# Optimization experiments

Hardware: AMD Instinct MI355X
Metric: run time of the kernel (lower is better)

The kernel has to match this reference:

```python
import jax, jax.numpy as jnp
import numpy as np

D = 256; H = 8; DK = D // H
NT, NW, ND = 2000, 50000, 20000
E_TT, E_WT, E_TD, E_WD = 128000, 256000, 320000, 320000
SQRT_DK = float(np.sqrt(DK))


def setup_inputs() -> dict:
    key = jax.random.key(0)
    ks = jax.random.split(key, 32)
    def nrm(i, shape, s=0.05):
        return jax.random.normal(ks[i], shape, jnp.float32) * s
    inp = {
        "feat_topic": nrm(0, (NT, D), 1.0),
        "feat_word": nrm(1, (NW, D), 1.0),
        "feat_doc": nrm(2, (ND, D), 1.0),
        "ht_prev": nrm(3, (NT, D), 1.0),
        # stacked per-ntype linears, index: 0=topic, 1=word, 2=doc
        "Wk": nrm(4, (3, D, D)), "bk": nrm(5, (3, D)),
        "Wq": nrm(6, (3, D, D)), "bq": nrm(7, (3, D)),
        "Wv": nrm(8, (3, D, D)), "bv": nrm(9, (3, D)),
        # a_linears, index: 0=topic, 1=doc
        "Wa": nrm(10, (2, D, D)), "ba": nrm(11, (2, D)),
        "ln_g": jnp.ones((2, D), jnp.float32),
        "ln_b": jnp.zeros((2, D), jnp.float32),
        "skip": jnp.ones((2,), jnp.float32),
        # RNNCell for topic
        "Wih": nrm(12, (D, D)), "Whh": nrm(13, (D, D)),
        "bih": nrm(14, (D,)), "bhh": nrm(15, (D,)),
        # relation params, index: 0=tt, 1=wt, 2=td, 3=wd
        "rel_pri": jnp.ones((4, H), jnp.float32),
        "rel_att": nrm(16, (4, H, DK, DK), 0.1),
        "rel_msg": nrm(17, (4, H, DK, DK), 0.1),
        "src_tt": jax.random.randint(ks[18], (E_TT,), 0, NT),
        "dst_tt": jnp.arange(E_TT, dtype=jnp.int32) % NT,
        "src_wt": jax.random.randint(ks[19], (E_WT,), 0, NW),
        "dst_wt": jnp.arange(E_WT, dtype=jnp.int32) % NT,
        "src_td": jax.random.randint(ks[20], (E_TD,), 0, NT),
        "dst_td": jnp.arange(E_TD, dtype=jnp.int32) % ND,
        "src_wd": jax.random.randint(ks[21], (E_WD,), 0, NW),
        "dst_wd": jnp.arange(E_WD, dtype=jnp.int32) % ND,
    }
    return inp


def _proj(x, W, b):
    return (x @ W + b).reshape(-1, H, DK)


def _layernorm(x, g, b):
    mu = x.mean(-1, keepdims=True)
    var = ((x - mu) ** 2).mean(-1, keepdims=True)
    return (x - mu) * jax.lax.rsqrt(var + 1e-5) * g + b


def _rel_message(k, v, q, src, dst, pri, A_att, A_msg, n_dst):
    # k,v: [N_src,H,DK]; q: [N_dst,H,DK]; per-edge gather-compute-scatter
    key = jnp.einsum('ehd,hdo->eho', k[src], A_att)          # [E,H,DK]
    att = (q[dst] * key).sum(-1) * pri / SQRT_DK             # [E,H]
    val = jnp.einsum('ehd,hdo->eho', v[src], A_msg)          # [E,H,DK]
    m = jax.ops.segment_max(att, dst, num_segments=n_dst)
    e = jnp.exp(att - m[dst])
    s = jax.ops.segment_sum(e, dst, num_segments=n_dst)
    a = e / s[dst]                                           # edge softmax per dst
    t = jax.ops.segment_sum(a[..., None] * val, dst, num_segments=n_dst)
    return jax.nn.relu(t.reshape(n_dst, D))


def reference(feat_topic, feat_word, feat_doc, ht_prev, Wk, bk, Wq, bq, Wv, bv,
              Wa, ba, ln_g, ln_b, skip, Wih, Whh, bih, bhh,
              rel_pri, rel_att, rel_msg,
              src_tt, dst_tt, src_wt, dst_wt, src_td, dst_td, src_wd, dst_wd):
    # ---- phase 1: messages into topic nodes (etypes tt, wt) ----
    k_t = _proj(feat_topic, Wk[0], bk[0]); v_t = _proj(feat_topic, Wv[0], bv[0])
    k_w = _proj(feat_word,  Wk[1], bk[1]); v_w = _proj(feat_word,  Wv[1], bv[1])
    q_t = _proj(feat_topic, Wq[0], bq[0])
    t_tt = _rel_message(k_t, v_t, q_t, src_tt, dst_tt, rel_pri[0], rel_att[0], rel_msg[0], NT)
    t_wt = _rel_message(k_w, v_w, q_t, src_wt, dst_wt, rel_pri[1], rel_att[1], rel_msg[1], NT)
    t_topic = 0.5 * (t_tt + t_wt)                            # cross_reducer='mean'
    alpha = jax.nn.sigmoid(skip[0])
    trans = t_topic @ Wa[0] + ba[0]
    mix = trans * alpha + feat_topic * (1.0 - alpha)
    h = jnp.tanh(mix @ Wih + bih + ht_prev @ Whh + bhh)      # RNNCell
    topic_out = _layernorm(h, ln_g[0], ln_b[0])
    # ---- phase 2: messages into doc nodes (etypes td, wd), topic uses updated feats ----
    k_t2 = _proj(topic_out, Wk[0], bk[0]); v_t2 = _proj(topic_out, Wv[0], bv[0])
    q_d = _proj(feat_doc, Wq[2], bq[2])
    t_td = _rel_message(k_t2, v_t2, q_d, src_td, dst_td, rel_pri[2], rel_att[2], rel_msg[2], ND)
    t_wd = _rel_message(k_w, v_w, q_d, src_wd, dst_wd, rel_pri[3], rel_att[3], rel_msg[3], ND)
    t_doc = 0.5 * (t_td + t_wd)
    alpha2 = jax.nn.sigmoid(skip[1])
    trans2 = t_doc @ Wa[1] + ba[1]
    mix2 = trans2 * alpha2 + feat_doc * (1.0 - alpha2)
    doc_out = _layernorm(mix2, ln_g[1], ln_b[1])
    return topic_out, doc_out
```

## Files before the change

### kernel.cpp

```cpp
#include <hip/hip_runtime.h>
#include <hip/hip_bf16.h>
#include <hip/hip_fp8.h>

typedef __attribute__((ext_vector_type(8))) short bf16x8;
typedef __attribute__((ext_vector_type(4))) float f32x4;
typedef __attribute__((ext_vector_type(2))) float f32x2;

constexpr int NT = 2000, NW = 50000, ND = 20000;
constexpr float INV_SQRT_DK = 0.17677669529663687f;

__device__ inline float bfu(unsigned short u) {
    return __uint_as_float(((unsigned int)u) << 16);
}
__device__ inline float blo(unsigned int u) { return __uint_as_float(u << 16); }
__device__ inline float bhi(unsigned int u) { return __uint_as_float(u & 0xffff0000u); }
__device__ inline short f2bf(float x) {
    __hip_bfloat16 h = __float2bfloat16(x);
    short s; __builtin_memcpy(&s, &h, 2); return s;
}

__device__ inline void dec4(unsigned int w, float* o) {
#if __has_builtin(__builtin_amdgcn_cvt_pk_f32_fp8)
    f32x2 a = __builtin_amdgcn_cvt_pk_f32_fp8(w, false);
    f32x2 b = __builtin_amdgcn_cvt_pk_f32_fp8(w, true);
    o[0] = a[0]; o[1] = a[1]; o[2] = b[0]; o[3] = b[1];
#else
    __hip_fp8_e4m3 t0, t1, t2, t3;
    t0.__x = (__hip_fp8_storage_t)(w & 0xff);
    t1.__x = (__hip_fp8_storage_t)((w >> 8) & 0xff);
    t2.__x = (__hip_fp8_storage_t)((w >> 16) & 0xff);
    t3.__x = (__hip_fp8_storage_t)((w >> 24) & 0xff);
    o[0] = (float)t0; o[1] = (float)t1; o[2] = (float)t2; o[3] = (float)t3;
#endif
}
__device__ inline unsigned char f2fp8(float v) {
#if __has_builtin(__builtin_amdgcn_cvt_pk_fp8_f32)
    return (unsigned char)(__builtin_amdgcn_cvt_pk_fp8_f32(v, v, 0u, false) & 0xff);
#else
    __hip_fp8_e4m3 h(v); return (unsigned char)h.__x;
#endif
}

__device__ inline void cstore(float* p, float v) { *p = v; }
__device__ inline void cstore(short* p, float v) { *p = f2bf(v); }
__device__ inline void cstore(unsigned char* p, float v) { *p = f2fp8(v); }

__device__ inline void cstore4(float* p, float4 v) {
    *reinterpret_cast<float4*>(p) = v;
}
__device__ inline void cstore4(short* p, float4 v) {
    short4 s; s.x = f2bf(v.x); s.y = f2bf(v.y); s.z = f2bf(v.z); s.w = f2bf(v.w);
    *reinterpret_cast<short4*>(p) = s;
}
__device__ inline void cstore4(unsigned char* p, float4 v) {
#if __has_builtin(__builtin_amdgcn_cvt_pk_fp8_f32)
    unsigned int w = __builtin_amdgcn_cvt_pk_fp8_f32(v.x, v.y, 0u, false);
    w = __builtin_amdgcn_cvt_pk_fp8_f32(v.z, v.w, w, true);
    *reinterpret_cast<unsigned int*>(p) = w;
#else
    p[0] = f2fp8(v.x); p[1] = f2fp8(v.y); p[2] = f2fp8(v.z); p[3] = f2fp8(v.w);
#endif
}

__device__ inline void gload16(const short* g, short* l) {
    __builtin_amdgcn_global_load_lds(
        (const __attribute__((address_space(1))) void*)g,
        (__attribute__((address_space(3))) void*)l, 16, 0, 0);
}

__device__ inline float dot32f8(const unsigned char* __restrict__ kp, const float* __restrict__ qh) {
    const uint4 u = *reinterpret_cast<const uint4*>(kp);
    const uint4 v = *reinterpret_cast<const uint4*>(kp + 16);
    const unsigned int ws[8] = {u.x, u.y, u.z, u.w, v.x, v.y, v.z, v.w};
    float d = 0.f;
    #pragma unroll
    for (int c = 0; c < 8; ++c) {
        float f[4];
        dec4(ws[c], f);
        d += qh[c * 4 + 0] * f[0] + qh[c * 4 + 1] * f[1]
           + qh[c * 4 + 2] * f[2] + qh[c * 4 + 3] * f[3];
    }
    return d;
}

__global__ __launch_bounds__(256) void fold_kernel(
    const float* __restrict__ Wk, const float* __restrict__ bk,
    const float* __restrict__ Wv, const float* __restrict__ bv,
    const float* __restrict__ rel_att, const float* __restrict__ rel_msg,
    short* __restrict__ B_t1, short* __restrict__ B_w, short* __restrict__ B_t2,
    float* __restrict__ bias_t1, float* __restrict__ bias_w, float* __restrict__ bias_t2)
{
    const int f = blockIdx.x >> 3, chunk = blockIdx.x & 7;
    const int rel = f >> 1, isV = f & 1;
    const int ntype = (rel == 1 || rel == 3) ? 1 : 0;
    const float* Wsrc = (isV ? Wv : Wk) + ntype * 65536;
    const float* bsrc = (isV ? bv : bk) + ntype * 256;
    const float* A    = (isV ? rel_msg : rel_att) + rel * 8192;
    short* wdst; float* bdst;
    switch (f) {
        case 0: wdst = B_t1 + 65536;     bdst = bias_t1 + 256; break;
        case 1: wdst = B_t1 + 2 * 65536; bdst = bias_t1 + 512; break;
        case 2: wdst = B_w;              bdst = bias_w;        break;
        case 3: wdst = B_w + 65536;      bdst = bias_w + 256;  break;
        case 4: wdst = B_t2;             bdst = bias_t2;       break;
        case 5: wdst = B_t2 + 65536;     bdst = bias_t2 + 256; break;
        case 6: wdst = B_w + 2 * 65536;  bdst = bias_w + 512;  break;
        default: wdst = B_w + 3 * 65536; bdst = bias_w + 768;  break;
    }
    __shared__ float Wsh[32][256];
    const int tid = threadIdx.x;
    for (int i = 0; i < 32; ++i)
        Wsh[i][tid] = Wsrc[(chunk * 32 + i) * 256 + tid];
    __syncthreads();
    const int h = tid >> 5, o = tid & 31;
    float a[32];
    #pragma unroll
    for (int d = 0; d < 32; ++d) a[d] = A[h * 1024 + d * 32 + o];
    short tmp[32];
    #pragma unroll
    for (int r = 0; r < 32; ++r) {
        float s = 0.f;
        #pragma unroll
        for (int d = 0; d < 32; ++d) s = fmaf(Wsh[r][(h << 5) + d], a[d], s);
        tmp[r] = f2bf(s);
    }
    short* wp = wdst + tid * 256 + chunk * 32;
    #pragma unroll
    for (int r8 = 0; r8 < 4; ++r8) {
        bf16x8 v;
        #pragma unroll
        for (int t = 0; t < 8; ++t) v[t] = tmp[r8 * 8 + t];
        *reinterpret_cast<bf16x8*>(wp + r8 * 8) = v;
    }
    if (chunk == 0) {
        float s = 0.f;
        #pragma unroll
        for (int d = 0; d < 32; ++d) s = fmaf(bsrc[(h << 5) + d], a[d], s);
        bdst[tid] = s;
    }
}

struct TransP { const float* s[6]; short* d[6]; };
__global__ __launch_bounds__(256) void wtrans6(TransP p) {
    const int m = blockIdx.y, n = blockIdx.x, k = threadIdx.x;
    p.d[m][n * 256 + k] = f2bf(p.s[m][k * 256 + n]);
}

__global__ void copy_bias(const float* __restrict__ s, float* __restrict__ d) {
    d[threadIdx.x] = s[threadIdx.x];
}

template <typename OutT, int EPI, int NI>
__device__ inline void epilogue(
    f32x4 (&acc)[NI][4], const float* __restrict__ bias, OutT* __restrict__ C,
    int M, int ldc, const float* __restrict__ extra,
    const float* __restrict__ skipv, int skipIdx,
    int row0, int col0, int wm, int wn, int r, int kb)
{
    float alpha = 0.f;
    if (EPI == 1) alpha = 1.f / (1.f + __expf(-skipv[skipIdx]));
    float4 b4[4];
    #pragma unroll
    for (int j = 0; j < 4; ++j)
        b4[j] = *reinterpret_cast<const float4*>(&bias[col0 + wn * 64 + j * 16 + kb * 4]);
    #pragma unroll
    for (int i = 0; i < NI; ++i) {
        const int rrow = row0 + wm * 64 + i * 16 + r;
        if (rrow >= M) continue;
        #pragma unroll
        for (int j = 0; j < 4; ++j) {
            const int cb = col0 + wn * 64 + j * 16 + kb * 4;
            float4 v;
            v.x = acc[i][j][0] + b4[j].x;
            v.y = acc[i][j][1] + b4[j].y;
            v.z = acc[i][j][2] + b4[j].z;
            v.w = acc[i][j][3] + b4[j].w;
            if (EPI == 1) {
                const float4 e = *reinterpret_cast<const float4*>(&extra[rrow * 256 + cb]);
                v.x = alpha * v.x + (1.f - alpha) * e.x;
                v.y = alpha * v.y + (1.f - alpha) * e.y;
                v.z = alpha * v.z + (1.f - alpha) * e.z;
                v.w = alpha * v.w + (1.f - alpha) * e.w;
            }
            if (EPI == 2) {
                const float4 e = *reinterpret_cast<const float4*>(&extra[rrow * 256 + cb]);
                v.x = tanhf(v.x + e.x);
                v.y = tanhf(v.y + e.y);
                v.z = tanhf(v.z + e.z);
                v.w = tanhf(v.w + e.w);
            }
            cstore4(C + rrow * ldc + cb, v);
        }
    }
}

template <bool XF32, typename OutT, int EPI, bool SWZ>
__global__ __launch_bounds__(256) void gemm_lds(
    const void* __restrict__ Xv, const short* __restrict__ Wt,
    const float* __restrict__ bias, OutT* __restrict__ C,
    int M, int ldc, const float* __restrict__ extra,
    const float* __restrict__ skipv, int skipIdx)
{
    __shared__ short As[128 * 64];
    __shared__ short Bs[128 * 64];
    int bxi = blockIdx.x, byi = blockIdx.y;
    if constexpr (SWZ) {
        const int h = bxi + (int)gridDim.x * byi;
        const int i = h >> 3;
        byi = (h & 7) + 8 * (i >> 3);
        bxi = i & 7;
        if (byi * 128 >= M) return;
    }
    const int tid = threadIdx.x;
    const int wave = tid >> 6, lane = tid & 63;
    const int wm = wave >> 1, wn = wave & 1;
    const int r = lane & 15, kb = lane >> 4;
    const int col0 = bxi * 128;
    const int row0 = byi * 128;

    const int l8 = lane >> 3;
    const int c8 = lane & 7;
    const int swz8 = c8 ^ l8;
    f32x4 acc[4][4] = {};

    for (int k0 = 0; k0 < 256; k0 += 64) {
        if (k0) __syncthreads();
        if constexpr (XF32) {
            #pragma unroll
            for (int q = 0; q < 4; ++q) {
                const int rl = wave * 32 + q * 8 + l8;
                const int grow = min(row0 + rl, M - 1);
                const float* xp = (const float*)Xv + grow * 256 + k0 + c8 * 8;
                const float4 x0 = *reinterpret_cast<const float4*>(xp);
                const float4 x1 = *reinterpret_cast<const float4*>(xp + 4);
                bf16x8 v;
                v[0] = f2bf(x0.x); v[1] = f2bf(x0.y); v[2] = f2bf(x0.z); v[3] = f2bf(x0.w);
                v[4] = f2bf(x1.x); v[5] = f2bf(x1.y); v[6] = f2bf(x1.z); v[7] = f2bf(x1.w);
                *reinterpret_cast<bf16x8*>(As + rl * 64 + swz8 * 8) = v;
            }
        } else {
            #pragma unroll
            for (int q = 0; q < 4; ++q) {
                const int rl = wave * 32 + q * 8 + l8;
                const int grow = min(row0 + rl, M - 1);
                gload16((const short*)Xv + grow * 256 + k0 + swz8 * 8,
                        As + (wave * 32 + q * 8) * 64);
            }
        }
        #pragma unroll
        for (int q = 0; q < 4; ++q) {
            const int cl = wave * 32 + q * 8 + l8;
            gload16(Wt + (col0 + cl) * 256 + k0 + swz8 * 8,
                    Bs + (wave * 32 + q * 8) * 64);
        }
        __syncthreads();
        #pragma unroll
        for (int s = 0; s < 2; ++s) {
            const int csw = ((kb + 4 * s) ^ (r & 7)) * 8;
            bf16x8 af[4], bw[4];
            #pragma unroll
            for (int i = 0; i < 4; ++i) {
                af[i] = *reinterpret_cast<const bf16x8*>(As + (wm * 64 + i * 16 + r) * 64 + csw);
                bw[i] = *reinterpret_cast<const bf16x8*>(Bs + (wn * 64 + i * 16 + r) * 64 + csw);
            }
            #pragma unroll
            for (int i = 0; i < 4; ++i)
                #pragma unroll
                for (int j = 0; j < 4; ++j)
                    acc[i][j] = __builtin_amdgcn_mfma_f32_16x16x32_bf16(bw[j], af[i], acc[i][j], 0, 0, 0);
        }
    }
    epilogue<OutT, EPI, 4>(acc, bias, C, M, ldc, extra, skipv, skipIdx,
                           row0, col0, wm, wn, r, kb);
}

__global__ __launch_bounds__(256) void gemm_qkv(
    const float* __restrict__ X, const short* __restrict__ Wt,
    const float* __restrict__ bias, short* __restrict__ Qo,
    unsigned char* __restrict__ KVo, int M)
{
    __shared__ short As[128 * 64];
    __shared__ short Bs[128 * 64];
    const int bxi = blockIdx.x, byi = blockIdx.y;
    const int tid = threadIdx.x;
    const int wave = tid >> 6, lane = tid & 63;
    const int wm = wave >> 1, wn = wave & 1;
    const int r = lane & 15, kb = lane >> 4;
    const int col0 = bxi * 128;
    const int row0 = byi * 128;

    const int l8 = lane >> 3;
    const int c8 = lane & 7;
    const int swz8 = c8 ^ l8;
    f32x4 acc[4][4] = {};

    for (int k0 = 0; k0 < 256; k0 += 64) {
        if (k0) __syncthreads();
        #pragma unroll
        for (int q = 0; q < 4; ++q) {
            const int rl = wave * 32 + q * 8 + l8;
            const int grow = min(row0 + rl, M - 1);
            const float* xp = X + grow * 256 + k0 + c8 * 8;
            const float4 x0 = *reinterpret_cast<const float4*>(xp);
            const float4 x1 = *reinterpret_cast<const float4*>(xp + 4);
            bf16x8 v;
            v[0] = f2bf(x0.x); v[1] = f2bf(x0.y); v[2] = f2bf(x0.z); v[3] = f2bf(x0.w);
            v[4] = f2bf(x1.x); v[5] = f2bf(x1.y); v[6] = f2bf(x1.z); v[7] = f2bf(x1.w);
            *reinterpret_cast<bf16x8*>(As + rl * 64 + swz8 * 8) = v;
        }
        #pragma unroll
        for (int q = 0; q < 4; ++q) {
            const int cl = wave * 32 + q * 8 + l8;
            gload16(Wt + (col0 + cl) * 256 + k0 + swz8 * 8,
                    Bs + (wave * 32 + q * 8) * 64);
        }
        __syncthreads();
        #pragma unroll
        for (int s = 0; s < 2; ++s) {
            const int csw = ((kb + 4 * s) ^ (r & 7)) * 8;
            bf16x8 af[4], bw[4];
            #pragma unroll
            for (int i = 0; i < 4; ++i) {
                af[i] = *reinterpret_cast<const bf16x8*>(As + (wm * 64 + i * 16 + r) * 64 + csw);
                bw[i] = *reinterpret_cast<const bf16x8*>(Bs + (wn * 64 + i * 16 + r) * 64 + csw);
            }
            #pragma unroll
            for (int i = 0; i < 4; ++i)
                #pragma unroll
                for (int j = 0; j < 4; ++j)
                    acc[i][j] = __builtin_amdgcn_mfma_f32_16x16x32_bf16(bw[j], af[i], acc[i][j], 0, 0, 0);
        }
    }

    float4 b4[4];
    #pragma unroll
    for (int j = 0; j < 4; ++j)
        b4[j] = *reinterpret_cast<const float4*>(&bias[col0 + wn * 64 + j * 16 + kb * 4]);
    #pragma unroll
    for (int i = 0; i < 4; ++i) {
        const int rrow = row0 + wm * 64 + i * 16 + r;
        if (rrow >= M) continue;
        #pragma unroll
        for (int j = 0; j < 4; ++j) {
            const int cb = col0 + wn * 64 + j * 16 + kb * 4;
            float4 v;
            v.x = acc[i][j][0] + b4[j].x;
            v.y = acc[i][j][1] + b4[j].y;
            v.z = acc[i][j][2] + b4[j].z;
            v.w = acc[i][j][3] + b4[j].w;
            if (bxi < 2) cstore4(Qo + rrow * 256 + cb, v);
            else         cstore4(KVo + rrow * 512 + (cb - 256), v);
        }
    }
}

template <bool XF32, typename OutT, int EPI, bool SWZ, bool SWAP>
__global__ __launch_bounds__(512) void gemm_w(
    const void* __restrict__ Xv, const short* __restrict__ Wt,
    const float* __restrict__ bias, OutT* __restrict__ C,
    int M, int ldc, const float* __restrict__ extra,
    const float* __restrict__ skipv, int skipIdx)
{
    __shared__ short As[256 * 64];
    __shared__ short Bs[128 * 64];
    int bxi = blockIdx.x, byi = blockIdx.y;
    if constexpr (SWZ) {
        const int h = bxi + (int)gridDim.x * byi;
        const int i = h >> 3;
        byi = (h & 7) + 8 * (i >> 3);
        bxi = i & 7;
        if (byi * 256 >= M) return;
    }
    const int tid = threadIdx.x;
    const int wave = tid >> 6, lane = tid & 63;
    const int wm = wave >> 1, wn = wave & 1;
    const int r = lane & 15, kb = lane >> 4;
    const int col0 = bxi * 128;
    const int row0 = byi * 256;

    const int l8 = lane >> 3;
    const int c8 = lane & 7;
    const int swz8 = c8 ^ l8;
    f32x4 acc[4][4] = {};

    for (int k0 = 0; k0 < 256; k0 += 64) {
        if (k0) __syncthreads();
        if constexpr (XF32) {
            #pragma unroll
            for (int q = 0; q < 4; ++q) {
                const int rl = wave * 32 + q * 8 + l8;
                const int grow = min(row0 + rl, M - 1);
                const float* xp = (const float*)Xv + grow * 256 + k0 + c8 * 8;
                const float4 x0 = *reinterpret_cast<const float4*>(xp);
                const float4 x1 = *reinterpret_cast<const float4*>(xp + 4);
                bf16x8 v;
                v[0] = f2bf(x0.x); v[1] = f2bf(x0.y); v[2] = f2bf(x0.z); v[3] = f2bf(x0.w);
                v[4] = f2bf(x1.x); v[5] = f2bf(x1.y); v[6] = f2bf(x1.z); v[7] = f2bf(x1.w);
                *reinterpret_cast<bf16x8*>(As + rl * 64 + swz8 * 8) = v;
            }
        } else {
            #pragma unroll
            for (int q = 0; q < 4; ++q) {
                const int rl = wave * 32 + q * 8 + l8;
                const int grow = min(row0 + rl, M - 1);
                gload16((const short*)Xv + grow * 256 + k0 + swz8 * 8,
                        As + (wave * 32 + q * 8) * 64);
            }
        }
        #pragma unroll
        for (int q = 0; q < 2; ++q) {
            const int cl = wave * 16 + q * 8 + l8;
            gload16(Wt + (col0 + cl) * 256 + k0 + swz8 * 8,
                    Bs + (wave * 16 + q * 8) * 64);
        }
        __syncthreads();
        #pragma unroll
        for (int s = 0; s < 2; ++s) {
            const int csw = ((kb + 4 * s) ^ (r & 7)) * 8;
            bf16x8 af[4], bw[4];
            #pragma unroll
            for (int i = 0; i < 4; ++i) {
                af[i] = *reinterpret_cast<const bf16x8*>(As + (wm * 64 + i * 16 + r) * 64 + csw);
                bw[i] = *reinterpret_cast<const bf16x8*>(Bs + (wn * 64 + i * 16 + r) * 64 + csw);
            }
            #pragma unroll
            for (int i = 0; i < 4; ++i)
                #pragma unroll
                for (int j = 0; j < 4; ++j) {
                    if constexpr (SWAP)
                        acc[i][j] = __builtin_amdgcn_mfma_f32_16x16x32_bf16(bw[j], af[i], acc[i][j], 0, 0, 0);
                    else
                        acc[i][j] = __builtin_amdgcn_mfma_f32_16x16x32_bf16(af[i], bw[j], acc[i][j], 0, 0, 0);
                }
        }
    }

    if constexpr (SWAP) {
        epilogue<OutT, EPI, 4>(acc, bias, C, M, ldc, extra, skipv, skipIdx,
                               row0, col0, wm, wn, r, kb);
    } else {
        float alpha = 0.f;
        if (EPI == 1) alpha = 1.f / (1.f + __expf(-skipv[skipIdx]));
        #pragma unroll
        for (int i = 0; i < 4; ++i) {
            #pragma unroll
            for (int j = 0; j < 4; ++j) {
                const int col = col0 + wn * 64 + j * 16 + r;
                const float bc = bias[col];
                #pragma unroll
                for (int t = 0; t < 4; ++t) {
                    const int rrow = row0 + wm * 64 + i * 16 + kb * 4 + t;
                    if (rrow < M) {
                        float v = acc[i][j][t] + bc;
                        if (EPI == 1) v = alpha * v + (1.f - alpha) * extra[rrow * 256 + col];
                        if (EPI == 2) v = tanhf(v + extra[rrow * 256 + col]);
                        cstore(C + rrow * ldc + col, v);
                    }
                }
            }
        }
    }
}

template <int NE>
__device__ inline void rel_scores_f8(const unsigned char* __restrict__ kv, int ld, int koff,
                                     const int* __restrict__ sidx, int off, float scale,
                                     const float* __restrict__ qh, float* __restrict__ sc,
                                     int g, int l)
{
    constexpr int NL = NE / 32;
    float att[NL];
    #pragma unroll
    for (int t = 0; t < NL; ++t)
        att[t] = dot32f8(kv + (size_t)sidx[off + l + 32 * t] * ld + koff + g * 32, qh) * scale;
    float m = att[0];
    #pragma unroll
    for (int t = 1; t < NL; ++t) m = fmaxf(m, att[t]);
    #pragma unroll
    for (int o = 16; o > 0; o >>= 1) m = fmaxf(m, __shfl_xor(m, o));
    float ex[NL], s = 0.f;
    #pragma unroll
    for (int t = 0; t < NL; ++t) { ex[t] = __expf(att[t] - m); s += ex[t]; }
    #pragma unroll
    for (int o = 16; o > 0; o >>= 1) s += __shfl_xor(s, o);
    const float inv = 1.f / s;
    #pragma unroll
    for (int t = 0; t < NL; ++t) sc[(off + l + 32 * t) * 9 + g] = ex[t] * inv;
}

template <int NEA, int NEB>
__global__ __launch_bounds__(256) void msg_k(
    const short* __restrict__ q, int ldq,
    const unsigned char* __restrict__ kvA, int ldA, int koffA, int voffA,
    const int* __restrict__ srcA,
    const unsigned char* __restrict__ kvB, int ldB, int koffB, int voffB,
    const int* __restrict__ srcB,
    const float* __restrict__ relPri, int relA, int relB,
    short* __restrict__ out, int n_dst)
{
    constexpr int NET = NEA + NEB;
    const int j = blockIdx.x, tid = threadIdx.x;
    __shared__ float qsh[256];
    __shared__ int sidx[NET];
    __shared__ float sc[NET * 9];
    __shared__ float ps[8][544];

    if (tid < 64) {
        const ushort4 u = *reinterpret_cast<const ushort4*>(
            (const unsigned short*)q + j * ldq + tid * 4);
        float4 f; f.x = bfu(u.x); f.y = bfu(u.y); f.z = bfu(u.z); f.w = bfu(u.w);
        *reinterpret_cast<float4*>(qsh + tid * 4) = f;
    }
    if (tid < NEA) sidx[tid] = srcA[j + tid * n_dst];
    else if (tid < NET) sidx[tid] = srcB[j + (tid - NEA) * n_dst];
    __syncthreads();

    const int g = tid >> 5, l = tid & 31;
    float qr[32];
    #pragma unroll
    for (int c = 0; c < 8; ++c) {
        const float4 v = *reinterpret_cast<const float4*>(qsh + g * 32 + c * 4);
        qr[c * 4] = v.x; qr[c * 4 + 1] = v.y; qr[c * 4 + 2] = v.z; qr[c * 4 + 3] = v.w;
    }

    if constexpr (NEA == 16 && NEB == 16) {
        const int isB = l >> 4;
        const unsigned char* base = isB ? kvB + koffB : kvA + koffA;
        const int ld = isB ? ldB : ldA;
        const float scale = relPri[(isB ? relB : relA) * 8 + g] * INV_SQRT_DK;
        const float att = dot32f8(base + (size_t)sidx[l] * ld + g * 32, qr) * scale;
        float m = att;
        #pragma unroll
        for (int o = 8; o > 0; o >>= 1) m = fmaxf(m, __shfl_xor(m, o));
        const float ex = __expf(att - m);
        float s = ex;
        #pragma unroll
        for (int o = 8; o > 0; o >>= 1) s += __shfl_xor(s, o);
        sc[l * 9 + g] = ex / s;
    } else {
        rel_scores_f8<NEA>(kvA, ldA, koffA, sidx, 0,
                           relPri[relA * 8 + g] * INV_SQRT_DK, qr, sc, g, l);
        rel_scores_f8<NEB>(kvB, ldB, koffB, sidx, NEA,
                           relPri[relB * 8 + g] * INV_SQRT_DK, qr, sc, g, l);
    }
    __syncthreads();

    const int ct16 = tid & 15;
    const int rel  = (tid >> 4) & 1;
    const int es   = tid >> 5;
    const int hh   = ct16 >> 1;
    const unsigned char* kvR = rel ? kvB : kvA;
    const int ldR   = rel ? ldB : ldA;
    const int voffR = rel ? voffB : voffA;
    const int offR  = rel ? NEA : 0;
    const int neR   = rel ? NEB : NEA;
    float acc[16] = {};
    for (int e = es; e < neR; e += 8) {
        const float w = sc[(offR + e) * 9 + hh];
        const uint4 u = *reinterpret_cast<const uint4*>(
            kvR + (size_t)sidx[offR + e] * ldR + voffR + ct16 * 16);
        float f[16];
        dec4(u.x, f); dec4(u.y, f + 4); dec4(u.z, f + 8); dec4(u.w, f + 12);
        #pragma unroll
        for (int k = 0; k < 16; ++k) acc[k] = fmaf(w, f[k], acc[k]);
    }
    {
        float* pp = &ps[es][rel * 272 + ct16 * 17];
        #pragma unroll
        for (int k = 0; k < 16; ++k) pp[k] = acc[k];
    }
    __syncthreads();

    const int ra = (tid >> 4) * 17 + (tid & 15);
    float rA = 0.f, rB = 0.f;
    #pragma unroll
    for (int e2 = 0; e2 < 8; ++e2) { rA += ps[e2][ra]; rB += ps[e2][272 + ra]; }
    const float val = 0.5f * (fmaxf(rA, 0.f) + fmaxf(rB, 0.f));
    unsigned short* ob = (unsigned short*)qsh;
    ob[tid] = (unsigned short)f2bf(val);
    __syncthreads();
    if (tid < 32) {
        const uint4 u = *reinterpret_cast<const uint4*>(ob + tid * 8);
        *reinterpret_cast<uint4*>((unsigned short*)out + j * 256 + tid * 8) = u;
    }
}

template <bool WB>
__global__ __launch_bounds__(256) void ln_k(
    float* __restrict__ data, const float* __restrict__ g,
    const float* __restrict__ b, int nrows, short* __restrict__ bfout)
{
    const int wid = threadIdx.x >> 6, lane = threadIdx.x & 63;
    const int row = blockIdx.x * 4 + wid;
    if (row >= nrows) return;
    float4 x = *reinterpret_cast<float4*>(data + row * 256 + lane * 4);
    float s  = x.x + x.y + x.z + x.w;
    float q2 = x.x * x.x + x.y * x.y + x.z * x.z + x.w * x.w;
    #pragma unroll
    for (int o = 32; o > 0; o >>= 1) { s += __shfl_xor(s, o); q2 += __shfl_xor(q2, o); }
    const float mu  = s * (1.f / 256.f);
    const float var = q2 * (1.f / 256.f) - mu * mu;
    const float rr = rsqrtf(var + 1e-5f);
    const float4 gg = *reinterpret_cast<const float4*>(g + lane * 4);
    const float4 bb = *reinterpret_cast<const float4*>(b + lane * 4);
    x.x = (x.x - mu) * rr * gg.x + bb.x;
    x.y = (x.y - mu) * rr * gg.y + bb.y;
    x.z = (x.z - mu) * rr * gg.z + bb.z;
    x.w = (x.w - mu) * rr * gg.w + bb.w;
    *reinterpret_cast<float4*>(data + row * 256 + lane * 4) = x;
    if (WB) {
        ushort4 u;
        u.x = (unsigned short)f2bf(x.x); u.y = (unsigned short)f2bf(x.y);
        u.z = (unsigned short)f2bf(x.z); u.w = (unsigned short)f2bf(x.w);
        *reinterpret_cast<ushort4*>((unsigned short*)bfout + row * 256 + lane * 4) = u;
    }
}

extern "C" void kernel_launch(void* const* d_in, const int* in_sizes, int n_in,
                              void* d_out, int out_size, void* d_ws, size_t ws_size,
                              hipStream_t stream)
{
    const float* feat_topic = (const float*)d_in[0];
    const float* feat_word  = (const float*)d_in[1];
    const float* feat_doc   = (const float*)d_in[2];
    const float* ht_prev    = (const float*)d_in[3];
    const float* Wk  = (const float*)d_in[4];
    const float* bk  = (const float*)d_in[5];
    const float* Wq  = (const float*)d_in[6];
    const float* bq  = (const float*)d_in[7];
    const float* Wv  = (const float*)d_in[8];
    const float* bv  = (const float*)d_in[9];
    const float* Wa  = (const float*)d_in[10];
    const float* ba  = (const float*)d_in[11];
    const float* ln_g = (const float*)d_in[12];
    const float* ln_b = (const float*)d_in[13];
    const float* skip = (const float*)d_in[14];
    const float* Wih  = (const float*)d_in[15];
    const float* Whh  = (const float*)d_in[16];
    const float* bih  = (const float*)d_in[17];
    const float* bhh  = (const float*)d_in[18];
    const float* rel_pri = (const float*)d_in[19];
    const float* rel_att = (const float*)d_in[20];
    const float* rel_msg = (const float*)d_in[21];
    const int* src_tt = (const int*)d_in[22];
    const int* src_wt = (const int*)d_in[24];
    const int* src_td = (const int*)d_in[26];
    const int* src_wd = (const int*)d_in[28];

    short* B_t1 = (short*)d_ws;
    short* B_w  = B_t1 + 196608;
    short* B_t2 = B_w + 262144;
    short* Wq2t = B_t2 + 131072;
    short* Whht = Wq2t + 65536;
    short* Wa0t = Whht + 65536;
    short* Wiht = Wa0t + 65536;
    short* Wa1t = Wiht + 65536;
    short* q_t  = Wa1t + 65536;
    unsigned char* kv1 = (unsigned char*)(q_t + 512000);
    unsigned char* w8  = kv1 + 1024000;
    unsigned char* kv2 = w8 + 51200000;
    short* qd   = (short*)(kv2 + 1024000);
    short* ttop = qd + 5120000;
    short* mixb = ttop + 512000;
    short* tdoc = mixb + 512000;
    short* xt2  = tdoc + 5120000;
    float* bias_t1 = (float*)(xt2 + 512000);
    float* bias_w  = bias_t1 + 768;
    float* bias_t2 = bias_w + 1024;
    float* r2      = bias_t2 + 512;

    float* out_topic = (float*)d_out;
    float* out_doc   = out_topic + NT * 256;

    fold_kernel<<<dim3(64), 256, 0, stream>>>(Wk, bk, Wv, bv, rel_att, rel_msg,
                                              B_t1, B_w, B_t2, bias_t1, bias_w, bias_t2);
    TransP tp;
    tp.s[0] = Wq;            tp.d[0] = B_t1;
    tp.s[1] = Wq + 131072;   tp.d[1] = Wq2t;
    tp.s[2] = Whh;           tp.d[2] = Whht;
    tp.s[3] = Wih;           tp.d[3] = Wiht;
    tp.s[4] = Wa;            tp.d[4] = Wa0t;
    tp.s[5] = Wa + 65536;    tp.d[5] = Wa1t;
    wtrans6<<<dim3(256, 6), 256, 0, stream>>>(tp);
    copy_bias<<<dim3(1), 256, 0, stream>>>(bq, bias_t1);

    gemm_w<true, unsigned char, 0, true, false><<<dim3(8, 200), 512, 0, stream>>>(
        feat_word, B_w, bias_w, w8, NW, 1024, nullptr, nullptr, 0);

    gemm_qkv<<<dim3(6, 16), 256, 0, stream>>>(
        feat_topic, B_t1, bias_t1, q_t, kv1, NT);
    gemm_w<true, short, 0, false, true><<<dim3(2, 79), 512, 0, stream>>>(
        feat_doc, Wq2t, bq + 512, qd, ND, 256, nullptr, nullptr, 0);
    gemm_lds<true, float, 0, false><<<dim3(2, 16), 256, 0, stream>>>(
        ht_prev, Whht, bhh, r2, NT, 256, nullptr, nullptr, 0);

    msg_k<64, 128><<<dim3(NT), 256, 0, stream>>>(
        q_t, 256,
        kv1, 512, 0, 256, src_tt,
        w8, 1024, 0, 256, src_wt,
        rel_pri, 0, 1, ttop, NT);

    gemm_lds<false, short, 1, false><<<dim3(2, 16), 256, 0, stream>>>(
        ttop, Wa0t, ba, mixb, NT, 256, feat_topic, skip, 0);
    gemm_lds<false, float, 2, false><<<dim3(2, 16), 256, 0, stream>>>(
        mixb, Wiht, bih, out_topic, NT, 256, r2, nullptr, 0);
    ln_k<true><<<dim3(500), 256, 0, stream>>>(out_topic, ln_g, ln_b, NT, xt2);

    gemm_lds<false, unsigned char, 0, false><<<dim3(4, 16), 256, 0, stream>>>(
        xt2, B_t2, bias_t2, kv2, NT, 512, nullptr, nullptr, 0);

    msg_k<16, 16><<<dim3(ND), 256, 0, stream>>>(
        qd, 256,
        kv2, 512, 0, 256, src_td,
        w8, 1024, 512, 768, src_wd,
        rel_pri, 2, 3, tdoc, ND);

    gemm_w<false, float, 1, false, true><<<dim3(2, 79), 512, 0, stream>>>(
        tdoc, Wa1t, ba + 256, out_doc, ND, 256, feat_doc, skip, 1);
    ln_k<false><<<dim3(5000), 256, 0, stream>>>(out_doc, ln_g + 256, ln_b + 256, ND, nullptr);
}
```

Measured before the change: 254.7 us.

## Pre-convert word features to bf16 and fold Whh GEMM into QKV launch

Adds a standalone kernel that converts feat_word from fp32 to bf16 once, so the large word-projection GEMM reads bf16 inputs through its non-converting path. It also merges the ht_prev@Whh GEMM into the topic QKV GEMM launch as two extra column-block groups, removing one small kernel launch. The conversion adds an extra full read and write pass over the 50000x256 word matrix, traded against cheaper A-loads in the GEMM. The merged launch shares tiles but branches on block index for inputs and outputs.

```diff
diff --git a/kernel.cpp b/kernel.cpp
--- a/kernel.cpp
+++ b/kernel.cpp
@@ -81,6 +81,20 @@
            + qh[c * 4 + 2] * f[2] + qh[c * 4 + 3] * f[3];
     }
     return d;
+}
+
+__global__ __launch_bounds__(256) void cvt_bf16(
+    const float* __restrict__ src, short* __restrict__ dst, int n8)
+{
+    const int i = blockIdx.x * 256 + threadIdx.x;
+    if (i >= n8) return;
+    const float* p = src + (long)i * 8;
+    const float4 x0 = *reinterpret_cast<const float4*>(p);
+    const float4 x1 = *reinterpret_cast<const float4*>(p + 4);
+    bf16x8 v;
+    v[0] = f2bf(x0.x); v[1] = f2bf(x0.y); v[2] = f2bf(x0.z); v[3] = f2bf(x0.w);
+    v[4] = f2bf(x1.x); v[5] = f2bf(x1.y); v[6] = f2bf(x1.z); v[7] = f2bf(x1.w);
+    *reinterpret_cast<bf16x8*>(dst + (long)i * 8) = v;
 }
 
 __global__ __launch_bounds__(256) void fold_kernel(
@@ -277,16 +291,22 @@
 __global__ __launch_bounds__(256) void gemm_qkv(
     const float* __restrict__ X, const short* __restrict__ Wt,
     const float* __restrict__ bias, short* __restrict__ Qo,
-    unsigned char* __restrict__ KVo, int M)
+    unsigned char* __restrict__ KVo, int M,
+    const float* __restrict__ X2, const short* __restrict__ Wt2,
+    const float* __restrict__ bias2, float* __restrict__ Ro)
 {
     __shared__ short As[128 * 64];
     __shared__ short Bs[128 * 64];
     const int bxi = blockIdx.x, byi = blockIdx.y;
+    const bool isR = bxi >= 6;
+    const float* Xp = isR ? X2 : X;
+    const short* Wp = isR ? Wt2 : Wt;
+    const float* bp = isR ? bias2 : bias;
+    const int colW = isR ? (bxi - 6) * 128 : bxi * 128;
     const int tid = threadIdx.x;
     const int wave = tid >> 6, lane = tid & 63;
     const int wm = wave >> 1, wn = wave & 1;
     const int r = lane & 15, kb = lane >> 4;
-    const int col0 = bxi * 128;
     const int row0 = byi * 128;
 
     const int l8 = lane >> 3;
@@ -300,7 +320,7 @@
         for (int q = 0; q < 4; ++q) {
             const int rl = wave * 32 + q * 8 + l8;
             const int grow = min(row0 + rl, M - 1);
-            const float* xp = X + grow * 256 + k0 + c8 * 8;
+            const float* xp = Xp + grow * 256 + k0 + c8 * 8;
             const float4 x0 = *reinterpret_cast<const float4*>(xp);
             const float4 x1 = *reinterpret_cast<const float4*>(xp + 4);
             bf16x8 v;
@@ -311,7 +331,7 @@
         #pragma unroll
         for (int q = 0; q < 4; ++q) {
             const int cl = wave * 32 + q * 8 + l8;
-            gload16(Wt + (col0 + cl) * 256 + k0 + swz8 * 8,
+            gload16(Wp + (colW + cl) * 256 + k0 + swz8 * 8,
                     Bs + (wave * 32 + q * 8) * 64);
         }
         __syncthreads();
@@ -335,21 +355,22 @@
     float4 b4[4];
     #pragma unroll
     for (int j = 0; j < 4; ++j)
-        b4[j] = *reinterpret_cast<const float4*>(&bias[col0 + wn * 64 + j * 16 + kb * 4]);
+        b4[j] = *reinterpret_cast<const float4*>(&bp[colW + wn * 64 + j * 16 + kb * 4]);
     #pragma unroll
     for (int i = 0; i < 4; ++i) {
         const int rrow = row0 + wm * 64 + i * 16 + r;
         if (rrow >= M) continue;
         #pragma unroll
         for (int j = 0; j < 4; ++j) {
-            const int cb = col0 + wn * 64 + j * 16 + kb * 4;
+            const int cb = colW + wn * 64 + j * 16 + kb * 4;
             float4 v;
             v.x = acc[i][j][0] + b4[j].x;
             v.y = acc[i][j][1] + b4[j].y;
             v.z = acc[i][j][2] + b4[j].z;
             v.w = acc[i][j][3] + b4[j].w;
-            if (bxi < 2) cstore4(Qo + rrow * 256 + cb, v);
-            else         cstore4(KVo + rrow * 512 + (cb - 256), v);
+            if (isR)          cstore4(Ro + rrow * 256 + cb, v);
+            else if (bxi < 2) cstore4(Qo + rrow * 256 + cb, v);
+            else              cstore4(KVo + rrow * 512 + (cb - 256), v);
         }
     }
 }
@@ -668,10 +689,12 @@
     float* bias_w  = bias_t1 + 768;
     float* bias_t2 = bias_w + 1024;
     float* r2      = bias_t2 + 512;
+    short* wfb     = (short*)(r2 + 512000);
 
     float* out_topic = (float*)d_out;
     float* out_doc   = out_topic + NT * 256;
 
+    cvt_bf16<<<dim3(6400), 256, 0, stream>>>(feat_word, wfb, NW * 256 / 8);
     fold_kernel<<<dim3(64), 256, 0, stream>>>(Wk, bk, Wv, bv, rel_att, rel_msg,
                                               B_t1, B_w, B_t2, bias_t1, bias_w, bias_t2);
     TransP tp;
@@ -684,15 +707,13 @@
     wtrans6<<<dim3(256, 6), 256, 0, stream>>>(tp);
     copy_bias<<<dim3(1), 256, 0, stream>>>(bq, bias_t1);
 
-    gemm_w<true, unsigned char, 0, true, false><<<dim3(8, 200), 512, 0, stream>>>(
-        feat_word, B_w, bias_w, w8, NW, 1024, nullptr, nullptr, 0);
-
-    gemm_qkv<<<dim3(6, 16), 256, 0, stream>>>(
-        feat_topic, B_t1, bias_t1, q_t, kv1, NT);
+    gemm_w<false, unsigned char, 0, true, false><<<dim3(8, 200), 512, 0, stream>>>(
+        wfb, B_w, bias_w, w8, NW, 1024, nullptr, nullptr, 0);
+
+    gemm_qkv<<<dim3(8, 16), 256, 0, stream>>>(
+        feat_topic, B_t1, bias_t1, q_t, kv1, NT, ht_prev, Whht, bhh, r2);
     gemm_w<true, short, 0, false, true><<<dim3(2, 79), 512, 0, stream>>>(
         feat_doc, Wq2t, bq + 512, qd, ND, 256, nullptr, nullptr, 0);
-    gemm_lds<true, float, 0, false><<<dim3(2, 16), 256, 0, stream>>>(
-        ht_prev, Whht, bhh, r2, NT, 256, nullptr, nullptr, 0);
 
     msg_k<64, 128><<<dim3(NT), 256, 0, stream>>>(
         q_t, 256,
```

After: 252.0 us. Within noise of the previous version (-1.1%).
